# Kernel optimization log

Measured on AMD Instinct MI355X. Metric: run time of the kernel, lower is better.

The kernel has to match this reference:

```python
import jax, jax.numpy as jnp
import numpy as np

B, L, DM, NL, ED, NS, DC, RK, CD, Q = 8, 1024, 256, 4, 512, 16, 4, 16, 64, 2


def _ln(x, g, b, eps=1e-5):
    m = x.mean(-1, keepdims=True)
    v = ((x - m) ** 2).mean(-1, keepdims=True)
    return (x - m) / jnp.sqrt(v + eps) * g + b


def setup_inputs() -> dict:
    key = jax.random.key(0)
    ks = jax.random.split(key, 32)
    rn = lambda k, sh, s=0.02: jax.random.normal(k, sh, jnp.float32) * s
    inp = {
        "tokens": jax.random.randint(ks[0], (B, L), 0, Q),
        "T": jax.random.uniform(ks[1], (B,), jnp.float32, 0.5, 2.0),
        "tok_embed": rn(ks[2], (Q, DM)),
        "pos_embed": rn(ks[3], (L, DM)),
        "tw1": rn(ks[4], (1, CD), 0.5),
        "tb1": rn(ks[5], (CD,), 0.1),
        "tw2": rn(ks[6], (CD, CD), 0.1),
        "tb2": rn(ks[7], (CD,), 0.1),
        "ag": jnp.ones((NL, DM), jnp.float32),
        "ab": jnp.zeros((NL, DM), jnp.float32),
        "apw": rn(ks[8], (NL, CD, 2 * DM), 0.01),
        "apb": jnp.zeros((NL, 2 * DM), jnp.float32),
        "in_w": rn(ks[9], (NL, DM, 2 * ED)),
        "conv_w": rn(ks[10], (NL, ED, DC), 0.2),
        "conv_b": jnp.zeros((NL, ED), jnp.float32),
        "xp_w": rn(ks[11], (NL, ED, RK + 2 * NS)),
        "dt_w": rn(ks[12], (NL, RK, ED), 0.1),
        "dt_b": rn(ks[13], (NL, ED), 0.1) - 4.0,  # softplus(~-4) gives small dt
        "A_log": jnp.log(jnp.broadcast_to(jnp.arange(1, NS + 1, dtype=jnp.float32), (NL, ED, NS))),
        "Dp": jnp.ones((NL, ED), jnp.float32),
        "out_w": rn(ks[14], (NL, ED, DM)),
        "fg": jnp.ones((DM,), jnp.float32),
        "fb": jnp.zeros((DM,), jnp.float32),
        "hw": rn(ks[15], (DM, Q)),
        "hb": jnp.zeros((Q,), jnp.float32),
    }
    return inp


def reference(tokens, T, tok_embed, pos_embed, tw1, tb1, tw2, tb2, ag, ab, apw, apb,
              in_w, conv_w, conv_b, xp_w, dt_w, dt_b, A_log, Dp, out_w, fg, fb, hw, hb):
    b, l = tokens.shape
    # shift-right token embedding + positional embedding
    emb = tok_embed[tokens]                                   # [B,L,DM]
    x = jnp.concatenate([jnp.zeros((b, 1, emb.shape[-1]), emb.dtype), emb[:, :-1]], axis=1)
    x = x + pos_embed[:l]
    # temperature conditioning MLP (exact GELU as in torch nn.GELU)
    h = jax.nn.gelu(T[:, None] @ tw1 + tb1, approximate=False)
    cond = h @ tw2 + tb2                                      # [B,CD]

    def comb(e1, e2):
        a1, b1 = e1
        a2, b2 = e2
        return a1 * a2, a2 * b1 + b2

    for i in range(NL):
        # AdaLN: (1 + scale) * LN(x) + shift
        ss = cond @ apw[i] + apb[i]                           # [B,2*DM]
        sc, sh = ss[:, :DM], ss[:, DM:]
        xn = (1.0 + sc[:, None, :]) * _ln(x, ag[i], ab[i]) + sh[:, None, :]
        # MambaBlock
        xz = xn @ in_w[i]                                     # [B,L,2*ED]
        xs, z = xz[..., :ED], xz[..., ED:]
        # causal depthwise conv1d (left-pad d_conv-1)
        xc = jnp.transpose(xs, (0, 2, 1))                     # [B,ED,L]
        xc = jax.lax.conv_general_dilated(xc, conv_w[i][:, None, :], (1,), [(DC - 1, 0)],
                                          feature_group_count=ED)
        xc = xc + conv_b[i][None, :, None]
        xs = jax.nn.silu(jnp.transpose(xc, (0, 2, 1)))        # [B,L,ED]
        # input-dependent SSM params
        xd = xs @ xp_w[i]                                     # [B,L,RK+2*NS]
        dlt = jax.nn.softplus(xd[..., :RK] @ dt_w[i] + dt_b[i])  # [B,L,ED]
        Bm, Cm = xd[..., RK:RK + NS], xd[..., RK + NS:]       # [B,L,NS]
        A = -jnp.exp(A_log[i])                                # [ED,NS]
        dA = jnp.exp(dlt[..., None] * A)                      # [B,L,ED,NS]
        dBx = (dlt * xs)[..., None] * Bm[:, :, None, :]       # [B,L,ED,NS]
        # selective scan: h_t = dA_t * h_{t-1} + dBx_t (parallel associative scan)
        _, hs = jax.lax.associative_scan(comb, (dA, dBx), axis=1)
        y = jnp.einsum('blen,bln->ble', hs, Cm) + Dp[i] * xs
        y = y * jax.nn.silu(z)
        x = x + y @ out_w[i]

    x = _ln(x, fg, fb)
    return x @ hw + hb                                        # [B,L,Q]
```

## Files before the change

kernel.cpp:

```cpp
#include <hip/hip_runtime.h>
#include <hip/hip_bf16.h>
#include <math.h>

#define B_   8
#define L_   1024
#define DM_  256
#define NL_  4
#define ED_  512
#define NS_  16
#define DC_  4
#define RK_  16
#define CD_  64
#define Q_   2

#define SEG_  32
#define SLEN_ 32

typedef __hip_bfloat16 bf16_t;
typedef __attribute__((ext_vector_type(8))) short short8;
typedef __attribute__((ext_vector_type(4))) float floatx4;

__device__ __forceinline__ float geluf(float x) {
    return 0.5f * x * (1.0f + erff(x * 0.70710678118654752f));
}
__device__ __forceinline__ float siluf(float x) {
    return x / (1.0f + __expf(-x));
}
__device__ __forceinline__ float softplus_fast(float x) {
    return (x > 20.0f) ? x : __logf(1.0f + __expf(x));
}
__device__ __forceinline__ float b2f(bf16_t v) { return __bfloat162float(v); }
__device__ __forceinline__ short f2bfbits(float v) {
    return __builtin_bit_cast(short, __float2bfloat16(v));
}

__global__ void k_transpose_all(const float* __restrict__ in_w,
                                const float* __restrict__ xp_w,
                                const float* __restrict__ out_w,
                                bf16_t* __restrict__ in_wT,
                                bf16_t* __restrict__ xp_wT,
                                bf16_t* __restrict__ out_wT) {
    __shared__ float t[32][33];
    int z = blockIdx.z;
    int which = z >> 2, layer = z & 3;
    const float* src; bf16_t* dst; int R, C;
    if (which == 0)      { R = DM_; C = 2 * ED_; src = in_w;  dst = in_wT;  }
    else if (which == 1) { R = ED_; C = 48;      src = xp_w;  dst = xp_wT;  }
    else                 { R = ED_; C = DM_;     src = out_w; dst = out_wT; }
    src += (size_t)layer * R * C;
    dst += (size_t)layer * R * C;
    int c0 = blockIdx.x * 32, r0 = blockIdx.y * 32;
    if (c0 >= C || r0 >= R) return;
    int tx = threadIdx.x & 31, ty = threadIdx.x >> 5;
    #pragma unroll
    for (int i = 0; i < 32; i += 8) {
        int r = r0 + ty + i, c = c0 + tx;
        t[ty + i][tx] = (r < R && c < C) ? src[(size_t)r * C + c] : 0.f;
    }
    __syncthreads();
    #pragma unroll
    for (int i = 0; i < 32; i += 8) {
        int c = c0 + ty + i, r = r0 + tx;
        if (c < C && r < R) dst[(size_t)c * R + r] = __float2bfloat16(t[tx][ty + i]);
    }
}

__global__ void k_embed(const int* __restrict__ tokens,
                        const float* __restrict__ tok_embed,
                        const float* __restrict__ pos_embed,
                        float* __restrict__ x) {
    int row = blockIdx.x;
    int d = threadIdx.x;
    int b = row / L_, l = row % L_;
    float v = pos_embed[l * DM_ + d];
    if (l > 0) {
        int tok = tokens[b * L_ + l - 1];
        v += tok_embed[tok * DM_ + d];
    }
    x[row * DM_ + d] = v;
}

__global__ void k_prep(const float* __restrict__ T,
                       const float* __restrict__ tw1, const float* __restrict__ tb1,
                       const float* __restrict__ tw2, const float* __restrict__ tb2,
                       const float* __restrict__ apw, const float* __restrict__ apb,
                       float* __restrict__ ss) {
    __shared__ float h[CD_], cnd[CD_];
    int b = blockIdx.x, layer = blockIdx.y;
    int j = threadIdx.x;
    if (j < CD_) h[j] = geluf(T[b] * tw1[j] + tb1[j]);
    __syncthreads();
    if (j < CD_) {
        float acc = tb2[j];
        #pragma unroll
        for (int c = 0; c < CD_; c++) acc += h[c] * tw2[c * CD_ + j];
        cnd[j] = acc;
    }
    __syncthreads();
    const float* w = apw + (size_t)layer * CD_ * 2 * DM_;
    float acc = apb[layer * 2 * DM_ + j];
    #pragma unroll
    for (int c = 0; c < CD_; c++) acc += cnd[c] * w[c * 2 * DM_ + j];
    ss[((size_t)layer * B_ + b) * 2 * DM_ + j] = acc;
}

__global__ __launch_bounds__(256) void k_ln_gemm_in(
        const float* __restrict__ x,
        const float* __restrict__ ag, const float* __restrict__ ab,
        const float* __restrict__ ss,
        const bf16_t* __restrict__ Bt,
        bf16_t* __restrict__ xz, int layer) {
    constexpr int BM = 64, BN = 128, K = 256, N = 2 * ED_;
    constexpr int TM = 2, TN = 4;
    __shared__ __align__(16) unsigned short sA[BM * 40];
    __shared__ __align__(16) unsigned short sB[BN * 40];
    __shared__ float s_mr[BM][2];
    __shared__ float s_prm[4 * DM_];

    const int tid = threadIdx.x;
    const int wave = tid >> 6, lane = tid & 63;
    const int lrow = lane & 15, lq = lane >> 4;
    const int bi = blockIdx.x;
    const int row0 = (bi & 127) * BM, col0 = (bi >> 7) * BN;
    const int b = row0 / L_;
    const int wm0 = (wave >> 1) * 32, wn0 = (wave & 1) * 64;

    {
        s_prm[tid]       = ag[layer * DM_ + tid];
        s_prm[256 + tid] = ab[layer * DM_ + tid];
        const float* ssl = ss + ((size_t)layer * B_ + b) * 2 * DM_;
        s_prm[512 + tid] = 1.0f + ssl[tid];
        s_prm[768 + tid] = ssl[DM_ + tid];
    }
    {
        int r = tid >> 2, part = tid & 3;
        const float* xr = x + (size_t)(row0 + r) * K + part * 64;
        float s = 0.f, q = 0.f;
        #pragma unroll
        for (int i = 0; i < 16; i++) {
            float4 v = *(const float4*)(xr + i * 4);
            s += (v.x + v.y) + (v.z + v.w);
            q += (v.x * v.x + v.y * v.y) + (v.z * v.z + v.w * v.w);
        }
        s += __shfl_xor(s, 1, 64);  q += __shfl_xor(q, 1, 64);
        s += __shfl_xor(s, 2, 64);  q += __shfl_xor(q, 2, 64);
        if (part == 0) {
            float mean = s * (1.0f / K);
            float var = q * (1.0f / K) - mean * mean;
            s_mr[r][0] = mean;
            s_mr[r][1] = rsqrtf(var + 1e-5f);
        }
    }

    floatx4 acc[TM][TN];
    #pragma unroll
    for (int i = 0; i < TM; i++)
        #pragma unroll
        for (int j = 0; j < TN; j++) acc[i][j] = (floatx4)0.0f;

    float4 raf[2];
    short8 rb[2];
    const int NKB = K / 32;
    {
        int m = tid >> 2, ko = (tid & 3) * 8;
        raf[0] = *(const float4*)(x + (size_t)(row0 + m) * K + ko);
        raf[1] = *(const float4*)(x + (size_t)(row0 + m) * K + ko + 4);
    }
    #pragma unroll
    for (int i = 0; i < 2; i++) {
        int v = tid + i * 256; int n = v >> 2, ko = (v & 3) * 8;
        rb[i] = *(const short8*)(Bt + (size_t)(col0 + n) * K + ko);
    }

    for (int kb = 0; kb < NKB; kb++) {
        __syncthreads();
        {
            int m = tid >> 2, ko = (tid & 3) * 8;
            int c0 = kb * 32 + ko;
            float mean = s_mr[m][0], rstd = s_mr[m][1];
            float av[8] = {raf[0].x, raf[0].y, raf[0].z, raf[0].w,
                           raf[1].x, raf[1].y, raf[1].z, raf[1].w};
            short8 o;
            #pragma unroll
            for (int j = 0; j < 8; j++) {
                int c = c0 + j;
                float ln = (av[j] - mean) * rstd * s_prm[c] + s_prm[256 + c];
                o[j] = f2bfbits(s_prm[512 + c] * ln + s_prm[768 + c]);
            }
            *(short8*)&sA[m * 40 + ko] = o;
        }
        #pragma unroll
        for (int i = 0; i < 2; i++) {
            int v = tid + i * 256; int n = v >> 2, ko = (v & 3) * 8;
            *(short8*)&sB[n * 40 + ko] = rb[i];
        }
        __syncthreads();
        if (kb + 1 < NKB) {
            int k0 = (kb + 1) * 32;
            {
                int m = tid >> 2, ko = (tid & 3) * 8;
                raf[0] = *(const float4*)(x + (size_t)(row0 + m) * K + k0 + ko);
                raf[1] = *(const float4*)(x + (size_t)(row0 + m) * K + k0 + ko + 4);
            }
            #pragma unroll
            for (int i = 0; i < 2; i++) {
                int v = tid + i * 256; int n = v >> 2, ko = (v & 3) * 8;
                rb[i] = *(const short8*)(Bt + (size_t)(col0 + n) * K + k0 + ko);
            }
        }
        short8 af[TM], bfr[TN];
        #pragma unroll
        for (int i = 0; i < TM; i++)
            af[i] = *(const short8*)&sA[(wm0 + i * 16 + lrow) * 40 + lq * 8];
        #pragma unroll
        for (int j = 0; j < TN; j++)
            bfr[j] = *(const short8*)&sB[(wn0 + j * 16 + lrow) * 40 + lq * 8];
        #pragma unroll
        for (int i = 0; i < TM; i++)
            #pragma unroll
            for (int j = 0; j < TN; j++)
                acc[i][j] = __builtin_amdgcn_mfma_f32_16x16x32_bf16(af[i], bfr[j], acc[i][j], 0, 0, 0);
    }

    #pragma unroll
    for (int i = 0; i < TM; i++) {
        int gr0 = row0 + wm0 + i * 16 + lq * 4;
        #pragma unroll
        for (int j = 0; j < TN; j++) {
            int gc = col0 + wn0 + j * 16 + lrow;
            #pragma unroll
            for (int r = 0; r < 4; r++) {
                float val = acc[i][j][r];
                if (gc >= ED_) val = siluf(val);
                xz[(size_t)(gr0 + r) * N + gc] = __float2bfloat16(val);
            }
        }
    }
}

__global__ __launch_bounds__(256) void k_conv_xp_dlt(
        const bf16_t* __restrict__ xz,
        const float* __restrict__ conv_w, const float* __restrict__ conv_b,
        const bf16_t* __restrict__ Bt,
        bf16_t* __restrict__ xs,
        float* __restrict__ xd,
        const float* __restrict__ dt_w, const float* __restrict__ dt_b,
        bf16_t* __restrict__ dlt, int layer) {
    constexpr int K = ED_;
    constexpr int BM = 16;
    __shared__ __align__(16) unsigned short sA[BM][520];
    __shared__ __align__(16) float s_rk[BM][20];

    const int tid = threadIdx.x;
    const int wave = tid >> 6, lane = tid & 63;
    const int lrow = lane & 15, lq = lane >> 4;
    const int row0 = blockIdx.x * BM;
    const int b = row0 >> 10;
    const int l0 = row0 & (L_ - 1);

    {
        const int e0 = tid * 2;
        float4 w0 = *(const float4*)(conv_w + ((size_t)layer * ED_ + e0) * DC_);
        float4 w1 = *(const float4*)(conv_w + ((size_t)layer * ED_ + e0 + 1) * DC_);
        float bias0 = conv_b[layer * ED_ + e0];
        float bias1 = conv_b[layer * ED_ + e0 + 1];
        const float wa0[4] = {w0.x, w0.y, w0.z, w0.w};
        const float wa1[4] = {w1.x, w1.y, w1.z, w1.w};
        float v0[BM + 3], v1[BM + 3];
        #pragma unroll
        for (int k = 0; k < BM + 3; k++) {
            int ll = l0 - 3 + k;
            if (ll >= 0) {
                __hip_bfloat162 v = *(const __hip_bfloat162*)(
                    xz + ((size_t)(b * L_ + ll)) * (2 * ED_) + e0);
                v0[k] = b2f(v.x); v1[k] = b2f(v.y);
            } else { v0[k] = 0.f; v1[k] = 0.f; }
        }
        #pragma unroll
        for (int j = 0; j < BM; j++) {
            float a0 = bias0, a1 = bias1;
            #pragma unroll
            for (int k = 0; k < DC_; k++) {
                a0 = fmaf(v0[j + k], wa0[k], a0);
                a1 = fmaf(v1[j + k], wa1[k], a1);
            }
            __hip_bfloat162 o;
            o.x = __float2bfloat16(siluf(a0));
            o.y = __float2bfloat16(siluf(a1));
            *(__hip_bfloat162*)(xs + (size_t)(row0 + j) * ED_ + e0) = o;
            *(__hip_bfloat162*)&sA[j][e0] = o;
        }
    }
    __syncthreads();

    const int nrow = (wave < 3) ? (wave * 16 + lrow) : lrow;
    const bf16_t* bptr = Bt + (size_t)nrow * K + lq * 8;
    floatx4 acc = (floatx4)0.0f;
    #pragma unroll
    for (int kb = 0; kb < K / 32; kb++) {
        short8 af = *(const short8*)&sA[lrow][kb * 32 + lq * 8];
        short8 bf = *(const short8*)(bptr + kb * 32);
        acc = __builtin_amdgcn_mfma_f32_16x16x32_bf16(af, bf, acc, 0, 0, 0);
    }

    if (wave == 1 || wave == 2) {
        int gc = wave * 16 + lrow;
        #pragma unroll
        for (int r = 0; r < 4; r++) {
            int gr = row0 + lq * 4 + r;
            xd[(size_t)gr * 48 + gc] = acc[r];
        }
    }
    if (wave == 0) {
        #pragma unroll
        for (int r = 0; r < 4; r++)
            s_rk[lq * 4 + r][lrow] = acc[r];
    }
    __syncthreads();

    const int e = 2 * tid;
    float2 wv[16];
    #pragma unroll
    for (int r = 0; r < RK_; r++)
        wv[r] = *(const float2*)(dt_w + ((size_t)layer * RK_ + r) * ED_ + e);
    float2 bb = *(const float2*)(dt_b + (size_t)layer * ED_ + e);
    #pragma unroll 4
    for (int row = 0; row < BM; row++) {
        float rk[16];
        #pragma unroll
        for (int q = 0; q < 4; q++)
            *(float4*)&rk[q * 4] = *(const float4*)&s_rk[row][q * 4];
        float a0 = bb.x, a1 = bb.y;
        #pragma unroll
        for (int r = 0; r < RK_; r++) {
            a0 = fmaf(rk[r], wv[r].x, a0);
            a1 = fmaf(rk[r], wv[r].y, a1);
        }
        __hip_bfloat162 o;
        o.x = __float2bfloat16(softplus_fast(a0));
        o.y = __float2bfloat16(softplus_fast(a1));
        *(__hip_bfloat162*)(dlt + (size_t)(row0 + row) * ED_ + e) = o;
    }
}


__global__ __launch_bounds__(256) void k_scan1(
        const bf16_t* __restrict__ dlt, const bf16_t* __restrict__ xs,
        const float* __restrict__ xd,
        const float* __restrict__ A_log,
        float* __restrict__ aprod, float* __restrict__ hend, int layer) {
    __shared__ float s_B[SLEN_][16];
    const int te = threadIdx.x;
    const int bi = blockIdx.x;
    const int seg = bi & (SEG_ - 1);
    const int eh  = (bi >> 5) & 1;
    const int b   = bi >> 6;
    const int e   = eh * 256 + te;
    const int rowbase = b * L_ + seg * SLEN_;

    if (te < SLEN_ * 4) {
        int flat = te * 4;
        int r = flat >> 4, c = flat & 15;
        *(float4*)&s_B[r][c] = *(const float4*)(xd + (size_t)(rowbase + r) * 48 + 16 + c);
    }

    float A[16];
    bool geo = true;
    {
        const float* ap = A_log + ((size_t)layer * ED_ + e) * NS_;
        #pragma unroll
        for (int n = 0; n < 16; n++) A[n] = -__expf(ap[n]);
        #pragma unroll
        for (int n = 1; n < 16; n++)
            geo = geo && (fabsf(A[n] - (float)(n + 1) * A[0]) <= 1e-3f * (float)(n + 1) * fabsf(A[0]));
    }

    float h[16];
    #pragma unroll
    for (int n = 0; n < 16; n++) h[n] = 0.f;
    float Pr = 1.0f;
    float P[16];
    #pragma unroll
    for (int n = 0; n < 16; n++) P[n] = 1.f;

    const bf16_t* dptr = dlt + (size_t)rowbase * ED_ + e;
    const bf16_t* xptr = xs  + (size_t)rowbase * ED_ + e;

    bf16_t dvb[8], xvb[8];
    #pragma unroll
    for (int j = 0; j < 8; j++) {
        dvb[j] = dptr[(size_t)j * ED_];
        xvb[j] = xptr[(size_t)j * ED_];
    }
    __syncthreads();

    for (int sub = 0; sub < SLEN_ / 8; sub++) {
        bf16_t dnx[8], xnx[8];
        if (sub < SLEN_ / 8 - 1) {
            const bf16_t* d2 = dptr + (size_t)(sub + 1) * 8 * ED_;
            const bf16_t* x2 = xptr + (size_t)(sub + 1) * 8 * ED_;
            #pragma unroll
            for (int j = 0; j < 8; j++) {
                dnx[j] = d2[(size_t)j * ED_];
                xnx[j] = x2[(size_t)j * ED_];
            }
        }
        if (geo) {
            #pragma unroll
            for (int j = 0; j < 8; j++) {
                int l = sub * 8 + j;
                float dv = b2f(dvb[j]), xv = b2f(xvb[j]);
                float dx = dv * xv;
                float Bv[16];
                #pragma unroll
                for (int q = 0; q < 4; q++)
                    *(float4*)&Bv[q * 4] = *(const float4*)&s_B[l][q * 4];
                float r = __expf(dv * A[0]);
                float r2 = r * r, r4 = r2 * r2;
                float a0 = r, a1 = r2, a2 = r2 * r, a3 = r4;
                #pragma unroll
                for (int q = 0; q < 4; q++) {
                    h[4*q+0] = fmaf(a0, h[4*q+0], dx * Bv[4*q+0]);
                    h[4*q+1] = fmaf(a1, h[4*q+1], dx * Bv[4*q+1]);
                    h[4*q+2] = fmaf(a2, h[4*q+2], dx * Bv[4*q+2]);
                    h[4*q+3] = fmaf(a3, h[4*q+3], dx * Bv[4*q+3]);
                    if (q < 3) { a0 *= r4; a1 *= r4; a2 *= r4; a3 *= r4; }
                }
                Pr *= r;
            }
        } else {
            #pragma unroll
            for (int j = 0; j < 8; j++) {
                int l = sub * 8 + j;
                float dv = b2f(dvb[j]), xv = b2f(xvb[j]);
                float dx = dv * xv;
                float Bv[16];
                #pragma unroll
                for (int q = 0; q < 4; q++)
                    *(float4*)&Bv[q * 4] = *(const float4*)&s_B[l][q * 4];
                #pragma unroll
                for (int n = 0; n < 16; n++) {
                    float a = __expf(dv * A[n]);
                    h[n] = fmaf(a, h[n], dx * Bv[n]);
                    P[n] *= a;
                }
            }
        }
        #pragma unroll
        for (int j = 0; j < 8; j++) { dvb[j] = dnx[j]; xvb[j] = xnx[j]; }
    }

    if (geo) {
        float p = Pr;
        #pragma unroll
        for (int n = 0; n < 16; n++) { P[n] = p; p *= Pr; }
    }
    #pragma unroll
    for (int n = 0; n < 16; n++) {
        size_t idx = ((((size_t)b * SEG_ + seg) << 4) + n) * ED_ + e;
        aprod[idx] = P[n];
        hend[idx]  = h[n];
    }
}

__global__ __launch_bounds__(256) void k_hinit(
        const float* __restrict__ aprod, const float* __restrict__ hend,
        float* __restrict__ hinit) {
    const int te = threadIdx.x;
    const int bi = blockIdx.x;
    const int n  = bi & 15;
    const int eh = (bi >> 4) & 1;
    const int b  = bi >> 5;
    const int e  = eh * 256 + te;
    float h = 0.f;
    for (int s = 0; s < SEG_; s++) {
        size_t idx = ((((size_t)b * SEG_ + s) << 4) + n) * ED_ + e;
        hinit[idx] = h;
        h = fmaf(aprod[idx], h, hend[idx]);
    }
}

__global__ __launch_bounds__(256) void k_scan3_outx(
        const bf16_t* __restrict__ dlt, const bf16_t* __restrict__ xs,
        const float* __restrict__ xd,
        const bf16_t* __restrict__ xz,
        const float* __restrict__ A_log, const float* __restrict__ Dp,
        const float* __restrict__ hinit,
        const bf16_t* __restrict__ Bt,
        float* __restrict__ x, int layer) {
    __shared__ float s_BC[SLEN_][32];
    __shared__ __align__(16) unsigned short sy[SLEN_][264];
    const int te = threadIdx.x;
    const int bi = blockIdx.x;
    const int seg = bi & (SEG_ - 1);
    const int eh  = (bi >> 5) & 1;
    const int b   = bi >> 6;
    const int e   = eh * 256 + te;
    const int rowbase = b * L_ + seg * SLEN_;

    {
        int flat = te * 4;
        int r = flat >> 5, c = flat & 31;
        *(float4*)&s_BC[r][c] = *(const float4*)(xd + (size_t)(rowbase + r) * 48 + 16 + c);
    }

    float A[16];
    bool geo = true;
    {
        const float* ap = A_log + ((size_t)layer * ED_ + e) * NS_;
        #pragma unroll
        for (int n = 0; n < 16; n++) A[n] = -__expf(ap[n]);
        #pragma unroll
        for (int n = 1; n < 16; n++)
            geo = geo && (fabsf(A[n] - (float)(n + 1) * A[0]) <= 1e-3f * (float)(n + 1) * fabsf(A[0]));
    }
    const float D = Dp[layer * ED_ + e];

    float h[16];
    {
        const size_t hb = (((size_t)b * SEG_ + seg) << 4) * ED_ + e;
        #pragma unroll
        for (int n = 0; n < 16; n++) h[n] = hinit[hb + (size_t)n * ED_];
    }

    const bf16_t* dptr = dlt + (size_t)rowbase * ED_ + e;
    const bf16_t* xptr = xs  + (size_t)rowbase * ED_ + e;
    const bf16_t* zptr = xz  + (size_t)rowbase * (2 * ED_) + ED_ + e;

    bf16_t dvb[8], xvb[8], zvb[8];
    #pragma unroll
    for (int j = 0; j < 8; j++) {
        dvb[j] = dptr[(size_t)j * ED_];
        xvb[j] = xptr[(size_t)j * ED_];
        zvb[j] = zptr[(size_t)j * (2 * ED_)];
    }
    __syncthreads();

    for (int sub = 0; sub < SLEN_ / 8; sub++) {
        bf16_t dnx[8], xnx[8], znx[8];
        if (sub < SLEN_ / 8 - 1) {
            const bf16_t* d2 = dptr + (size_t)(sub + 1) * 8 * ED_;
            const bf16_t* x2 = xptr + (size_t)(sub + 1) * 8 * ED_;
            const bf16_t* z2 = zptr + (size_t)(sub + 1) * 8 * (2 * ED_);
            #pragma unroll
            for (int j = 0; j < 8; j++) {
                dnx[j] = d2[(size_t)j * ED_];
                xnx[j] = x2[(size_t)j * ED_];
                znx[j] = z2[(size_t)j * (2 * ED_)];
            }
        }
        if (geo) {
            #pragma unroll
            for (int j = 0; j < 8; j++) {
                int l = sub * 8 + j;
                float dv = b2f(dvb[j]), xv = b2f(xvb[j]);
                float dx = dv * xv;
                float Bv[16], Cv[16];
                #pragma unroll
                for (int q = 0; q < 4; q++) {
                    *(float4*)&Bv[q * 4] = *(const float4*)&s_BC[l][q * 4];
                    *(float4*)&Cv[q * 4] = *(const float4*)&s_BC[l][16 + q * 4];
                }
                float r = __expf(dv * A[0]);
                float r2 = r * r, r4 = r2 * r2;
                float a0 = r, a1 = r2, a2 = r2 * r, a3 = r4;
                float y0 = D * xv, y1 = 0.f, y2 = 0.f, y3 = 0.f;
                #pragma unroll
                for (int q = 0; q < 4; q++) {
                    h[4*q+0] = fmaf(a0, h[4*q+0], dx * Bv[4*q+0]);
                    h[4*q+1] = fmaf(a1, h[4*q+1], dx * Bv[4*q+1]);
                    h[4*q+2] = fmaf(a2, h[4*q+2], dx * Bv[4*q+2]);
                    h[4*q+3] = fmaf(a3, h[4*q+3], dx * Bv[4*q+3]);
                    y0 = fmaf(Cv[4*q+0], h[4*q+0], y0);
                    y1 = fmaf(Cv[4*q+1], h[4*q+1], y1);
                    y2 = fmaf(Cv[4*q+2], h[4*q+2], y2);
                    y3 = fmaf(Cv[4*q+3], h[4*q+3], y3);
                    if (q < 3) { a0 *= r4; a1 *= r4; a2 *= r4; a3 *= r4; }
                }
                float yv = (y0 + y1) + (y2 + y3);
                sy[l][te] = (unsigned short)f2bfbits(yv * b2f(zvb[j]));
            }
        } else {
            #pragma unroll
            for (int j = 0; j < 8; j++) {
                int l = sub * 8 + j;
                float dv = b2f(dvb[j]), xv = b2f(xvb[j]);
                float dx = dv * xv;
                float Bv[16], Cv[16];
                #pragma unroll
                for (int q = 0; q < 4; q++) {
                    *(float4*)&Bv[q * 4] = *(const float4*)&s_BC[l][q * 4];
                    *(float4*)&Cv[q * 4] = *(const float4*)&s_BC[l][16 + q * 4];
                }
                float y0 = D * xv, y1 = 0.f, y2 = 0.f, y3 = 0.f;
                #pragma unroll
                for (int n = 0; n < 16; n++) {
                    float a = __expf(dv * A[n]);
                    h[n] = fmaf(a, h[n], dx * Bv[n]);
                    float t = Cv[n] * h[n];
                    if ((n & 3) == 0) y0 += t;
                    else if ((n & 3) == 1) y1 += t;
                    else if ((n & 3) == 2) y2 += t;
                    else y3 += t;
                }
                float yv = (y0 + y1) + (y2 + y3);
                sy[l][te] = (unsigned short)f2bfbits(yv * b2f(zvb[j]));
            }
        }
        #pragma unroll
        for (int j = 0; j < 8; j++) { dvb[j] = dnx[j]; xvb[j] = xnx[j]; zvb[j] = znx[j]; }
    }
    __syncthreads();

    {
        const int wave = te >> 6, lane = te & 63;
        const int lrow = lane & 15, lq = lane >> 4;
        const int ct = wave;
        floatx4 acc[2][4];
        #pragma unroll
        for (int mt = 0; mt < 2; mt++)
            #pragma unroll
            for (int t = 0; t < 4; t++) acc[mt][t] = (floatx4)0.0f;
        #pragma unroll 2
        for (int kb = 0; kb < 8; kb++) {
            short8 af0 = *(const short8*)&sy[lrow][kb * 32 + lq * 8];
            short8 af1 = *(const short8*)&sy[16 + lrow][kb * 32 + lq * 8];
            #pragma unroll
            for (int t = 0; t < 4; t++) {
                short8 bf = *(const short8*)(
                    Bt + (size_t)(ct * 64 + t * 16 + lrow) * ED_ + eh * 256 + kb * 32 + lq * 8);
                acc[0][t] = __builtin_amdgcn_mfma_f32_16x16x32_bf16(af0, bf, acc[0][t], 0, 0, 0);
                acc[1][t] = __builtin_amdgcn_mfma_f32_16x16x32_bf16(af1, bf, acc[1][t], 0, 0, 0);
            }
        }
        #pragma unroll
        for (int mt = 0; mt < 2; mt++) {
            #pragma unroll
            for (int t = 0; t < 4; t++) {
                int gc = ct * 64 + t * 16 + lrow;
                #pragma unroll
                for (int r = 0; r < 4; r++) {
                    int gr = rowbase + mt * 16 + lq * 4 + r;
                    atomicAdd(&x[(size_t)gr * DM_ + gc], acc[mt][t][r]);
                }
            }
        }
    }
}

__global__ void k_final(const float* __restrict__ x,
                        const float* __restrict__ fg, const float* __restrict__ fb,
                        const float* __restrict__ hw, const float* __restrict__ hb,
                        float* __restrict__ out) {
    int lane = threadIdx.x & 63, w = threadIdx.x >> 6;
    int row = blockIdx.x * 4 + w;
    const float* xr = x + (size_t)row * DM_;
    float v[4];
    #pragma unroll
    for (int k = 0; k < 4; k++) v[k] = xr[lane + 64 * k];
    float s = (v[0] + v[1]) + (v[2] + v[3]);
    float q = (v[0] * v[0] + v[1] * v[1]) + (v[2] * v[2] + v[3] * v[3]);
    #pragma unroll
    for (int off = 32; off > 0; off >>= 1) {
        s += __shfl_xor(s, off, 64);
        q += __shfl_xor(q, off, 64);
    }
    float mean = s * (1.0f / DM_);
    float var = q * (1.0f / DM_) - mean * mean;
    float rstd = rsqrtf(var + 1e-5f);
    float s0 = 0.f, s1 = 0.f;
    #pragma unroll
    for (int k = 0; k < 4; k++) {
        int c = lane + 64 * k;
        float xf = (v[k] - mean) * rstd * fg[c] + fb[c];
        s0 += xf * hw[c * Q_ + 0];
        s1 += xf * hw[c * Q_ + 1];
    }
    #pragma unroll
    for (int off = 32; off > 0; off >>= 1) {
        s0 += __shfl_xor(s0, off, 64);
        s1 += __shfl_xor(s1, off, 64);
    }
    if (lane == 0) {
        out[row * Q_ + 0] = s0 + hb[0];
        out[row * Q_ + 1] = s1 + hb[1];
    }
}

extern "C" void kernel_launch(void* const* d_in, const int* in_sizes, int n_in,
                              void* d_out, int out_size, void* d_ws, size_t ws_size,
                              hipStream_t stream) {
    const int*   tokens    = (const int*)d_in[0];
    const float* T         = (const float*)d_in[1];
    const float* tok_embed = (const float*)d_in[2];
    const float* pos_embed = (const float*)d_in[3];
    const float* tw1       = (const float*)d_in[4];
    const float* tb1       = (const float*)d_in[5];
    const float* tw2       = (const float*)d_in[6];
    const float* tb2       = (const float*)d_in[7];
    const float* ag        = (const float*)d_in[8];
    const float* ab        = (const float*)d_in[9];
    const float* apw       = (const float*)d_in[10];
    const float* apb       = (const float*)d_in[11];
    const float* in_w      = (const float*)d_in[12];
    const float* conv_w    = (const float*)d_in[13];
    const float* conv_b    = (const float*)d_in[14];
    const float* xp_w      = (const float*)d_in[15];
    const float* dt_w      = (const float*)d_in[16];
    const float* dt_b      = (const float*)d_in[17];
    const float* A_log     = (const float*)d_in[18];
    const float* Dp        = (const float*)d_in[19];
    const float* out_w     = (const float*)d_in[20];
    const float* fg        = (const float*)d_in[21];
    const float* fb        = (const float*)d_in[22];
    const float* hw        = (const float*)d_in[23];
    const float* hb        = (const float*)d_in[24];
    float* out = (float*)d_out;

    const int ROWS = B_ * L_;

    char* p = (char*)d_ws;
    float*  x      = (float*)p;   p += (size_t)ROWS * DM_ * 4;
    bf16_t* xz     = (bf16_t*)p;  p += (size_t)ROWS * 2 * ED_ * 2;
    bf16_t* xs     = (bf16_t*)p;  p += (size_t)ROWS * ED_ * 2;
    float*  xd     = (float*)p;   p += (size_t)ROWS * 48 * 4;
    bf16_t* dlt    = (bf16_t*)p;  p += (size_t)ROWS * ED_ * 2;
    float*  ss     = (float*)p;   p += (size_t)NL_ * B_ * 2 * DM_ * 4;
    float*  aprod  = (float*)p;   p += (size_t)B_ * SEG_ * NS_ * ED_ * 4;
    float*  hendb  = (float*)p;   p += (size_t)B_ * SEG_ * NS_ * ED_ * 4;
    float*  hinit  = (float*)p;   p += (size_t)B_ * SEG_ * NS_ * ED_ * 4;
    bf16_t* in_wT  = (bf16_t*)p;  p += (size_t)NL_ * 2 * ED_ * DM_ * 2;
    bf16_t* xp_wT  = (bf16_t*)p;  p += (size_t)NL_ * 48 * ED_ * 2;
    bf16_t* out_wT = (bf16_t*)p;  p += (size_t)NL_ * DM_ * ED_ * 2;

    k_transpose_all<<<dim3(32, 16, 12), 256, 0, stream>>>(
        in_w, xp_w, out_w, in_wT, xp_wT, out_wT);
    k_prep<<<dim3(B_, NL_), 2 * DM_, 0, stream>>>(T, tw1, tb1, tw2, tb2, apw, apb, ss);
    k_embed<<<ROWS, DM_, 0, stream>>>(tokens, tok_embed, pos_embed, x);

    for (int i = 0; i < NL_; i++) {
        k_ln_gemm_in<<<1024, 256, 0, stream>>>(
            x, ag, ab, ss, in_wT + (size_t)i * 2 * ED_ * DM_, xz, i);
        k_conv_xp_dlt<<<ROWS / 16, 256, 0, stream>>>(
            xz, conv_w, conv_b, xp_wT + (size_t)i * 48 * ED_, xs, xd,
            dt_w, dt_b, dlt, i);
        k_scan1<<<B_ * 2 * SEG_, 256, 0, stream>>>(dlt, xs, xd, A_log, aprod, hendb, i);
        k_hinit<<<B_ * 2 * NS_, 256, 0, stream>>>(aprod, hendb, hinit);
        k_scan3_outx<<<B_ * 2 * SEG_, 256, 0, stream>>>(
            dlt, xs, xd, xz, A_log, Dp, hinit,
            out_wT + (size_t)i * DM_ * ED_, x, i);
    }

    k_final<<<ROWS / 4, 256, 0, stream>>>(x, fg, fb, hw, hb, out);
}
```

Baseline: 449.5 us.

## Split LayerNorm+modulation out of in-proj GEMM and widen hinit grid

Moves the LayerNorm and FiLM modulation into a standalone per-row kernel that writes a bf16 normalized activation buffer. The in-projection GEMM then reads bf16 A directly with a 128x64 tile instead of recomputing row stats and normalizing fp32 inside every column tile. This removes redundant LN work repeated across 8 column blocks, at the cost of one extra launch and a bf16 round trip through memory. The hinit kernel is also relaunched with 128-thread blocks and twice as many blocks to spread the sequential segment loop over more CUs.

```diff
diff --git a/kernel.cpp b/kernel.cpp
--- a/kernel.cpp
+++ b/kernel.cpp
@@ -104,109 +104,98 @@
     ss[((size_t)layer * B_ + b) * 2 * DM_ + j] = acc;
 }
 
-__global__ __launch_bounds__(256) void k_ln_gemm_in(
+__global__ __launch_bounds__(256) void k_ln_mod(
         const float* __restrict__ x,
         const float* __restrict__ ag, const float* __restrict__ ab,
         const float* __restrict__ ss,
-        const bf16_t* __restrict__ Bt,
-        bf16_t* __restrict__ xz, int layer) {
-    constexpr int BM = 64, BN = 128, K = 256, N = 2 * ED_;
-    constexpr int TM = 2, TN = 4;
+        bf16_t* __restrict__ xn, int layer) {
+    int lane = threadIdx.x & 63, w = threadIdx.x >> 6;
+    int row = blockIdx.x * 4 + w;
+    int b = row >> 10;
+    const float* xr = x + (size_t)row * DM_;
+    float v[4];
+    #pragma unroll
+    for (int k = 0; k < 4; k++) v[k] = xr[lane + 64 * k];
+    float s = (v[0] + v[1]) + (v[2] + v[3]);
+    float q = (v[0] * v[0] + v[1] * v[1]) + (v[2] * v[2] + v[3] * v[3]);
+    #pragma unroll
+    for (int off = 32; off > 0; off >>= 1) {
+        s += __shfl_xor(s, off, 64);
+        q += __shfl_xor(q, off, 64);
+    }
+    float mean = s * (1.0f / DM_);
+    float var = q * (1.0f / DM_) - mean * mean;
+    float rstd = rsqrtf(var + 1e-5f);
+    const float* ssl = ss + ((size_t)layer * B_ + b) * 2 * DM_;
+    #pragma unroll
+    for (int k = 0; k < 4; k++) {
+        int c = lane + 64 * k;
+        float ln = (v[k] - mean) * rstd * ag[layer * DM_ + c] + ab[layer * DM_ + c];
+        float val = (1.0f + ssl[c]) * ln + ssl[DM_ + c];
+        xn[(size_t)row * DM_ + c] = __float2bfloat16(val);
+    }
+}
+
+__global__ __launch_bounds__(256) void k_gemm_in(
+        const bf16_t* __restrict__ A, const bf16_t* __restrict__ Bt,
+        bf16_t* __restrict__ xz) {
+    constexpr int BM = 128, BN = 64, K = 256, N = 2 * ED_;
+    constexpr int TM = 4, TN = 2;
     __shared__ __align__(16) unsigned short sA[BM * 40];
     __shared__ __align__(16) unsigned short sB[BN * 40];
-    __shared__ float s_mr[BM][2];
-    __shared__ float s_prm[4 * DM_];
 
     const int tid = threadIdx.x;
     const int wave = tid >> 6, lane = tid & 63;
     const int lrow = lane & 15, lq = lane >> 4;
+    const int nrt = (B_ * L_) / BM;
     const int bi = blockIdx.x;
-    const int row0 = (bi & 127) * BM, col0 = (bi >> 7) * BN;
-    const int b = row0 / L_;
-    const int wm0 = (wave >> 1) * 32, wn0 = (wave & 1) * 64;
-
+    const int row0 = (bi % nrt) * BM, col0 = (bi / nrt) * BN;
+    const int wm0 = (wave >> 1) * 64;
+    const int wn0 = (wave & 1) * 32;
+
+    floatx4 acc[TM][TN];
+    #pragma unroll
+    for (int i = 0; i < TM; i++)
+        #pragma unroll
+        for (int j = 0; j < TN; j++) acc[i][j] = (floatx4)0.0f;
+
+    short8 ra[2], rb;
+    const int NKB = K / 32;
+
+    #pragma unroll
+    for (int i = 0; i < 2; i++) {
+        int v = tid + i * 256;
+        int m = v >> 2, ko = (v & 3) * 8;
+        ra[i] = *(const short8*)(A + (size_t)(row0 + m) * K + ko);
+    }
     {
-        s_prm[tid]       = ag[layer * DM_ + tid];
-        s_prm[256 + tid] = ab[layer * DM_ + tid];
-        const float* ssl = ss + ((size_t)layer * B_ + b) * 2 * DM_;
-        s_prm[512 + tid] = 1.0f + ssl[tid];
-        s_prm[768 + tid] = ssl[DM_ + tid];
-    }
-    {
-        int r = tid >> 2, part = tid & 3;
-        const float* xr = x + (size_t)(row0 + r) * K + part * 64;
-        float s = 0.f, q = 0.f;
-        #pragma unroll
-        for (int i = 0; i < 16; i++) {
-            float4 v = *(const float4*)(xr + i * 4);
-            s += (v.x + v.y) + (v.z + v.w);
-            q += (v.x * v.x + v.y * v.y) + (v.z * v.z + v.w * v.w);
-        }
-        s += __shfl_xor(s, 1, 64);  q += __shfl_xor(q, 1, 64);
-        s += __shfl_xor(s, 2, 64);  q += __shfl_xor(q, 2, 64);
-        if (part == 0) {
-            float mean = s * (1.0f / K);
-            float var = q * (1.0f / K) - mean * mean;
-            s_mr[r][0] = mean;
-            s_mr[r][1] = rsqrtf(var + 1e-5f);
-        }
-    }
-
-    floatx4 acc[TM][TN];
-    #pragma unroll
-    for (int i = 0; i < TM; i++)
-        #pragma unroll
-        for (int j = 0; j < TN; j++) acc[i][j] = (floatx4)0.0f;
-
-    float4 raf[2];
-    short8 rb[2];
-    const int NKB = K / 32;
-    {
-        int m = tid >> 2, ko = (tid & 3) * 8;
-        raf[0] = *(const float4*)(x + (size_t)(row0 + m) * K + ko);
-        raf[1] = *(const float4*)(x + (size_t)(row0 + m) * K + ko + 4);
-    }
-    #pragma unroll
-    for (int i = 0; i < 2; i++) {
-        int v = tid + i * 256; int n = v >> 2, ko = (v & 3) * 8;
-        rb[i] = *(const short8*)(Bt + (size_t)(col0 + n) * K + ko);
+        int n = tid >> 2, ko = (tid & 3) * 8;
+        rb = *(const short8*)(Bt + (size_t)(col0 + n) * K + ko);
     }
 
     for (int kb = 0; kb < NKB; kb++) {
         __syncthreads();
+        #pragma unroll
+        for (int i = 0; i < 2; i++) {
+            int v = tid + i * 256;
+            int m = v >> 2, ko = (v & 3) * 8;
+            *(short8*)&sA[m * 40 + ko] = ra[i];
+        }
         {
-            int m = tid >> 2, ko = (tid & 3) * 8;
-            int c0 = kb * 32 + ko;
-            float mean = s_mr[m][0], rstd = s_mr[m][1];
-            float av[8] = {raf[0].x, raf[0].y, raf[0].z, raf[0].w,
-                           raf[1].x, raf[1].y, raf[1].z, raf[1].w};
-            short8 o;
-            #pragma unroll
-            for (int j = 0; j < 8; j++) {
-                int c = c0 + j;
-                float ln = (av[j] - mean) * rstd * s_prm[c] + s_prm[256 + c];
-                o[j] = f2bfbits(s_prm[512 + c] * ln + s_prm[768 + c]);
-            }
-            *(short8*)&sA[m * 40 + ko] = o;
-        }
-        #pragma unroll
-        for (int i = 0; i < 2; i++) {
-            int v = tid + i * 256; int n = v >> 2, ko = (v & 3) * 8;
-            *(short8*)&sB[n * 40 + ko] = rb[i];
+            int n = tid >> 2, ko = (tid & 3) * 8;
+            *(short8*)&sB[n * 40 + ko] = rb;
         }
         __syncthreads();
         if (kb + 1 < NKB) {
             int k0 = (kb + 1) * 32;
-            {
-                int m = tid >> 2, ko = (tid & 3) * 8;
-                raf[0] = *(const float4*)(x + (size_t)(row0 + m) * K + k0 + ko);
-                raf[1] = *(const float4*)(x + (size_t)(row0 + m) * K + k0 + ko + 4);
-            }
             #pragma unroll
             for (int i = 0; i < 2; i++) {
-                int v = tid + i * 256; int n = v >> 2, ko = (v & 3) * 8;
-                rb[i] = *(const short8*)(Bt + (size_t)(col0 + n) * K + k0 + ko);
-            }
+                int v = tid + i * 256;
+                int m = v >> 2, ko = (v & 3) * 8;
+                ra[i] = *(const short8*)(A + (size_t)(row0 + m) * K + k0 + ko);
+            }
+            int n = tid >> 2, ko = (tid & 3) * 8;
+            rb = *(const short8*)(Bt + (size_t)(col0 + n) * K + k0 + ko);
         }
         short8 af[TM], bfr[TN];
         #pragma unroll
@@ -463,15 +452,15 @@
     }
 }
 
-__global__ __launch_bounds__(256) void k_hinit(
+__global__ __launch_bounds__(128) void k_hinit(
         const float* __restrict__ aprod, const float* __restrict__ hend,
         float* __restrict__ hinit) {
     const int te = threadIdx.x;
     const int bi = blockIdx.x;
     const int n  = bi & 15;
-    const int eh = (bi >> 4) & 1;
-    const int b  = bi >> 5;
-    const int e  = eh * 256 + te;
+    const int eq = (bi >> 4) & 3;
+    const int b  = bi >> 6;
+    const int e  = eq * 128 + te;
     float h = 0.f;
     for (int s = 0; s < SEG_; s++) {
         size_t idx = ((((size_t)b * SEG_ + s) << 4) + n) * ED_ + e;
@@ -721,6 +710,7 @@
 
     char* p = (char*)d_ws;
     float*  x      = (float*)p;   p += (size_t)ROWS * DM_ * 4;
+    bf16_t* xn     = (bf16_t*)p;  p += (size_t)ROWS * DM_ * 2;
     bf16_t* xz     = (bf16_t*)p;  p += (size_t)ROWS * 2 * ED_ * 2;
     bf16_t* xs     = (bf16_t*)p;  p += (size_t)ROWS * ED_ * 2;
     float*  xd     = (float*)p;   p += (size_t)ROWS * 48 * 4;
@@ -739,13 +729,14 @@
     k_embed<<<ROWS, DM_, 0, stream>>>(tokens, tok_embed, pos_embed, x);
 
     for (int i = 0; i < NL_; i++) {
-        k_ln_gemm_in<<<1024, 256, 0, stream>>>(
-            x, ag, ab, ss, in_wT + (size_t)i * 2 * ED_ * DM_, xz, i);
+        k_ln_mod<<<ROWS / 4, 256, 0, stream>>>(x, ag, ab, ss, xn, i);
+        k_gemm_in<<<1024, 256, 0, stream>>>(
+            xn, in_wT + (size_t)i * 2 * ED_ * DM_, xz);
         k_conv_xp_dlt<<<ROWS / 16, 256, 0, stream>>>(
             xz, conv_w, conv_b, xp_wT + (size_t)i * 48 * ED_, xs, xd,
             dt_w, dt_b, dlt, i);
         k_scan1<<<B_ * 2 * SEG_, 256, 0, stream>>>(dlt, xs, xd, A_log, aprod, hendb, i);
-        k_hinit<<<B_ * 2 * NS_, 256, 0, stream>>>(aprod, hendb, hinit);
+        k_hinit<<<B_ * 4 * NS_, 128, 0, stream>>>(aprod, hendb, hinit);
         k_scan3_outx<<<B_ * 2 * SEG_, 256, 0, stream>>>(
             dlt, xs, xd, xz, A_log, Dp, hinit,
             out_wT + (size_t)i * DM_ * ED_, x, i);
```

New measurement: 428.5 us. 1.05x faster.
